# Optimization experiments

Measured on AMD Instinct MI355X. Metric: run time of the kernel, lower is better.

## Reference

```python
import jax, jax.numpy as jnp
import numpy as np
from jax import lax

DEPTH, HEADS, DH, DIM, M, V, NUM_EMB, D_VQ = 6, 8, 64, 512, 256, 523, 512, 64


def _ln(x, g, b):
    mu = jnp.mean(x, -1, keepdims=True)
    var = jnp.var(x, -1, keepdims=True)
    return (x - mu) * lax.rsqrt(var + 1e-5) * g + b


def _softmax_kernel(data, proj, is_query):
    # FAVOR+ positive softmax features (performer-pytorch softmax_kernel)
    dn = data * (data.shape[-1] ** -0.25)
    dd = jnp.einsum('bhld,md->bhlm', dn, proj)
    diag = 0.5 * jnp.sum(dn * dn, axis=-1, keepdims=True)
    mx = jnp.max(dd, axis=-1, keepdims=True) if is_query else jnp.max(dd)
    return jnp.exp(dd - diag - lax.stop_gradient(mx)) * (proj.shape[0] ** -0.5) + 1e-4


def _causal_linear_attn(qp, kp, v):
    # out_t = qp_t . cumsum_t(kp v^T) / (qp_t . cumsum_t(kp))
    kc = jnp.cumsum(kp, axis=2)
    den = jnp.einsum('bhlm,bhlm->bhl', qp, kc)
    kv = jnp.cumsum(jnp.einsum('bhlm,bhld->bhlmd', kp, v), axis=2)
    return jnp.einsum('bhlm,bhlmd->bhld', qp, kv) / den[..., None]


def _vq_encode(_x, conv1_w, conv1_b, conv2_w, conv2_b, codebook):
    dn = ('NCDHW', 'OIDHW', 'NCDHW')
    h = lax.conv_general_dilated(_x, conv1_w, (2, 2, 2), [(1, 1)] * 3, dimension_numbers=dn)
    h = jax.nn.relu(h + conv1_b[None, :, None, None, None])
    h = lax.conv_general_dilated(h, conv2_w, (2, 2, 2), [(1, 1)] * 3, dimension_numbers=dn)
    h = h + conv2_b[None, :, None, None, None]                 # [N, D, 4,4,4]
    z = jnp.transpose(h, (0, 2, 3, 4, 1))                      # [N, 4,4,4, D]
    flat = z.reshape(-1, z.shape[-1])
    d2 = (jnp.sum(flat * flat, 1, keepdims=True)
          - 2.0 * flat @ codebook.T
          + jnp.sum(codebook * codebook, 1)[None, :])
    inds = jnp.argmin(d2, axis=1).astype(jnp.int32)
    return inds.reshape(z.shape[:4])                           # [N, 4,4,4]


def _performer_loss(seq, tok_emb, pos_emb, proj, ln1_g, ln1_b, wq, wk, wv, wo, bo,
                    ln2_g, ln2_b, ff1_w, ff1_b, ff2_w, ff2_b, lnf_g, lnf_b,
                    logits_w, logits_b):
    inp, tgt = seq[:, :-1], seq[:, 1:]
    b, L = inp.shape
    h = tok_emb[inp] + pos_emb[:L][None]
    split = lambda t: jnp.transpose(t.reshape(b, L, HEADS, DH), (0, 2, 1, 3))
    for l in range(DEPTH):
        x1 = _ln(h, ln1_g[l], ln1_b[l])
        q, k, v = split(x1 @ wq[l]), split(x1 @ wk[l]), split(x1 @ wv[l])
        qp = _softmax_kernel(q, proj[l], True)
        kp = _softmax_kernel(k, proj[l], False)
        o = _causal_linear_attn(qp, kp, v)
        o = jnp.transpose(o, (0, 2, 1, 3)).reshape(b, L, DIM)
        h = h + o @ wo[l] + bo[l]
        x2 = _ln(h, ln2_g[l], ln2_b[l])
        h = h + jax.nn.gelu(x2 @ ff1_w[l] + ff1_b[l]) @ ff2_w[l] + ff2_b[l]
    h = _ln(h, lnf_g, lnf_b)
    logits = h @ logits_w + logits_b
    lp = jax.nn.log_softmax(logits, axis=-1)
    nll = -jnp.take_along_axis(lp, tgt[..., None], axis=-1)[..., 0]
    return jnp.mean(nll)


def setup_inputs() -> dict:
    key = jax.random.key(0)
    ks = jax.random.split(key, 24)
    n = lambda k, sh, s=0.02: (jax.random.normal(k, sh) * s).astype(jnp.float32)
    bs = 16
    return {
        'x': jax.random.normal(ks[0], (bs, 1, 16, 16, 16), jnp.float32),
        'xn': jax.random.normal(ks[1], (bs, 1, 1, 16, 16, 16), jnp.float32),
        'i': jax.random.randint(ks[2], (bs, 3), 0, V, jnp.int32),
        # frozen VQ-VAE
        'conv1_w': n(ks[3], (32, 1, 4, 4, 4), 0.1), 'conv1_b': jnp.zeros((32,), jnp.float32),
        'conv2_w': n(ks[4], (D_VQ, 32, 4, 4, 4), 0.05), 'conv2_b': jnp.zeros((D_VQ,), jnp.float32),
        'codebook': jax.random.normal(ks[5], (NUM_EMB, D_VQ), jnp.float32),
        # FAVOR+ random-feature projections (non-trainable buffer)
        'proj': jax.random.normal(ks[6], (DEPTH, M, DH), jnp.float32),
        # performer params
        'tok_emb': n(ks[7], (V, DIM)), 'pos_emb': n(ks[8], (131, DIM)),
        'ln1_g': jnp.ones((DEPTH, DIM), jnp.float32), 'ln1_b': jnp.zeros((DEPTH, DIM), jnp.float32),
        'wq': n(ks[9], (DEPTH, DIM, DIM)), 'wk': n(ks[10], (DEPTH, DIM, DIM)),
        'wv': n(ks[11], (DEPTH, DIM, DIM)), 'wo': n(ks[12], (DEPTH, DIM, DIM)),
        'bo': jnp.zeros((DEPTH, DIM), jnp.float32),
        'ln2_g': jnp.ones((DEPTH, DIM), jnp.float32), 'ln2_b': jnp.zeros((DEPTH, DIM), jnp.float32),
        'ff1_w': n(ks[13], (DEPTH, DIM, 4 * DIM)), 'ff1_b': jnp.zeros((DEPTH, 4 * DIM), jnp.float32),
        'ff2_w': n(ks[14], (DEPTH, 4 * DIM, DIM)), 'ff2_b': jnp.zeros((DEPTH, DIM), jnp.float32),
        'lnf_g': jnp.ones((DIM,), jnp.float32), 'lnf_b': jnp.zeros((DIM,), jnp.float32),
        'logits_w': n(ks[15], (DIM, V)), 'logits_b': jnp.zeros((V,), jnp.float32),
    }


def reference(x, xn, i, conv1_w, conv1_b, conv2_w, conv2_b, codebook, proj,
              tok_emb, pos_emb, ln1_g, ln1_b, wq, wk, wv, wo, bo, ln2_g, ln2_b,
              ff1_w, ff1_b, ff2_w, ff2_b, lnf_g, lnf_b, logits_w, logits_b):
    bs = x.shape[0]
    _xn = xn.reshape((-1,) + xn.shape[2:])            # (b n) c x y z
    _x = jnp.concatenate([x, _xn], axis=0)
    inds = _vq_encode(_x, conv1_w, conv1_b, conv2_w, conv2_b, codebook)
    inds_i = inds[:bs].reshape(bs, -1)                # b (x y z)
    inds_r = inds[bs:].reshape(bs, -1)                # b (n x y z)
    seq = jnp.concatenate([i.astype(jnp.int32), inds_r, inds_i], axis=1)  # [b, 131]
    return _performer_loss(seq, tok_emb, pos_emb, proj, ln1_g, ln1_b, wq, wk, wv, wo,
                           bo, ln2_g, ln2_b, ff1_w, ff1_b, ff2_w, ff2_b,
                           lnf_g, lnf_b, logits_w, logits_b)
```

## Files before the change

kernel.cpp:

```cpp
#include <hip/hip_runtime.h>

#define SEQL 130
#define LSEQ 131
#define DIMM 512
#define NHEADS 8
#define MF 256
#define VSZ 523
#define NROWS (16*SEQL)
#define NBH (16*NHEADS)
#define NBHL (NBH*SEQL)
#define QSEG 1064960

typedef __attribute__((ext_vector_type(8))) short short8;
typedef __attribute__((ext_vector_type(8))) unsigned short us8;
typedef __attribute__((ext_vector_type(4))) unsigned short us4;
typedef __attribute__((ext_vector_type(4))) float f32x4;

__device__ __forceinline__ unsigned short f2bf(float f){
  unsigned int u = __float_as_uint(f);
  u += 0x7fffu + ((u>>16)&1u);
  return (unsigned short)(u>>16);
}
__device__ __forceinline__ float bf2f(unsigned short h){
  return __uint_as_float(((unsigned int)h)<<16);
}
__device__ __forceinline__ float gelu_f(float x){
  float x3 = x*x*x;
  return 0.5f*x*(1.f+tanhf(0.7978845608028654f*(x+0.044715f*x3)));
}
__device__ __forceinline__ unsigned enc_max(float f){
  unsigned u = __float_as_uint(f);
  return (u & 0x80000000u) ? ~u : (u | 0x80000000u);
}
__device__ __forceinline__ float dec_max(unsigned k){
  unsigned u = (k>>31) ? (k & 0x7fffffffu) : ~k;
  return __uint_as_float(u);
}
__device__ __forceinline__ float blk_sum(float v){
  #pragma unroll
  for(int off=32;off;off>>=1) v += __shfl_xor(v,off);
  __shared__ float tmp_s[4];
  int t=threadIdx.x;
  if((t&63)==0) tmp_s[t>>6]=v;
  __syncthreads();
  v = tmp_s[0]+tmp_s[1]+tmp_s[2]+tmp_s[3];
  __syncthreads();
  return v;
}
__device__ __forceinline__ float blk_max(float v){
  #pragma unroll
  for(int off=32;off;off>>=1) v = fmaxf(v,__shfl_xor(v,off));
  __shared__ float tmp_m[4];
  int t=threadIdx.x;
  if((t&63)==0) tmp_m[t>>6]=v;
  __syncthreads();
  v = fmaxf(fmaxf(tmp_m[0],tmp_m[1]),fmaxf(tmp_m[2],tmp_m[3]));
  __syncthreads();
  return v;
}
__device__ __forceinline__ int tok_at(const int* __restrict__ iarr,
    const int* __restrict__ inds, int b, int p){
  if(p<3)  return iarr[b*3+p];
  if(p<67) return inds[(16+b)*64 + (p-3)];
  return inds[b*64 + (p-67)];
}

__global__ __launch_bounds__(256) void conv1_k(const float* __restrict__ x,
    const float* __restrict__ xn, const float* __restrict__ w,
    const float* __restrict__ bias, float* __restrict__ out){
  int idx = blockIdx.x*256 + threadIdx.x;
  if(idx >= 32*32*8*8*8) return;
  int ow = idx & 7, oh = (idx>>3)&7, od = (idx>>6)&7, oc = (idx>>9)&31, n = idx>>14;
  const float* xp = (n<16) ? (x + n*4096) : (xn + (n-16)*4096);
  const float* wp = w + oc*64;
  float acc = bias[oc];
  #pragma unroll
  for(int kd=0;kd<4;kd++){ int id = od*2-1+kd; if((unsigned)id>=16u) continue;
    #pragma unroll
    for(int kh=0;kh<4;kh++){ int ih = oh*2-1+kh; if((unsigned)ih>=16u) continue;
      #pragma unroll
      for(int kw=0;kw<4;kw++){ int iw = ow*2-1+kw; if((unsigned)iw>=16u) continue;
        acc += xp[(id*16+ih)*16+iw]*wp[(kd*4+kh)*4+kw];
      }}}
  out[idx] = fmaxf(acc,0.f);
}

__global__ __launch_bounds__(512) void conv2_k(const float* __restrict__ c1,
    const float* __restrict__ w, const float* __restrict__ bias,
    float* __restrict__ out){
  __shared__ float in_s[32][4][120];
  int od = blockIdx.x, n = blockIdx.y, ocg = blockIdx.z;
  int t = threadIdx.x;
  float4* zf = (float4*)&in_s[0][0][0];
  #pragma unroll
  for(int j=0;j<8;j++){
    int idx = t + 512*j;
    if(idx < 3840) zf[idx] = make_float4(0.f,0.f,0.f,0.f);
  }
  __syncthreads();
  #pragma unroll
  for(int j=0;j<2;j++){
    int ridx = t + 512*j;
    int ic = ridx>>5, rem = ridx&31;
    int kd = rem>>3, ih = rem&7;
    int id = od*2 - 1 + kd;
    if((unsigned)id < 8u){
      const float* src = c1 + (size_t)(n*32+ic)*512 + id*64 + ih*8;
      float4 a = *(const float4*)src;
      float4 b = *(const float4*)(src+4);
      float* dst = &in_s[ic][kd][(ih+1)*12 + 1];
      dst[0]=a.x; dst[1]=a.y; dst[2]=a.z; dst[3]=a.w;
      dst[4]=b.x; dst[5]=b.y; dst[6]=b.z; dst[7]=b.w;
    }
  }
  __syncthreads();
  int oc = ocg*32 + (t>>4);
  int oh = (t>>2)&3, ow = t&3;
  float acc = bias[oc];
  for(int ic=0; ic<32; ic++){
    #pragma unroll
    for(int kd=0;kd<4;kd++){
      #pragma unroll
      for(int kh=0;kh<4;kh++){
        f32x4 wv = *(const f32x4*)(w + ((size_t)(oc*32+ic)*64 + (kd*4+kh)*4));
        const float* base = &in_s[ic][kd][(oh*2+kh)*12 + ow*2];
        acc += wv[0]*base[0] + wv[1]*base[1] + wv[2]*base[2] + wv[3]*base[3];
      }
    }
  }
  out[(size_t)(n*64+oc)*64 + od*16 + oh*4 + ow] = acc;
}

__global__ __launch_bounds__(256) void vq_k(const float* __restrict__ c2,
    const float* __restrict__ cb, int* __restrict__ inds){
  int nf = blockIdx.x;
  int nb = nf>>6, sp = nf&63;
  __shared__ float z[64];
  int t = threadIdx.x;
  if(t<64) z[t] = c2[(nb*64+t)*64 + sp];
  __syncthreads();
  float best = 3.0e38f; int bi = 0;
  for(int j=t; j<512; j+=256){
    const float* cr = cb + j*64;
    float dot=0.f, nn=0.f;
    #pragma unroll 8
    for(int d=0;d<64;d++){ float cv=cr[d]; dot += z[d]*cv; nn += cv*cv; }
    float dist = nn - 2.f*dot;
    if(dist < best){ best=dist; bi=j; }
  }
  #pragma unroll
  for(int off=32;off;off>>=1){
    float ob = __shfl_down(best,off); int oi = __shfl_down(bi,off);
    if(ob<best || (ob==best && oi<bi)){ best=ob; bi=oi; }
  }
  __shared__ float rb[4]; __shared__ int ri[4];
  if((t&63)==0){ rb[t>>6]=best; ri[t>>6]=bi; }
  __syncthreads();
  if(t==0){
    for(int wv=1;wv<4;wv++){ if(rb[wv]<best || (rb[wv]==best && ri[wv]<bi)){ best=rb[wv]; bi=ri[wv]; } }
    inds[nf]=bi;
  }
}

__global__ __launch_bounds__(256) void embed_k(const int* __restrict__ iarr,
    const int* __restrict__ inds, const float* __restrict__ tok,
    const float* __restrict__ pos, float* __restrict__ h){
  int idx = blockIdx.x*256 + threadIdx.x;
  int c = idx & 511; int row = idx >> 9;
  int b = row/SEQL, l = row - b*SEQL;
  int tk = tok_at(iarr, inds, b, l);
  h[idx] = tok[tk*DIMM + c] + pos[l*DIMM + c];
}

__global__ __launch_bounds__(256) void ln_k(const float* __restrict__ in,
    const float* __restrict__ g, const float* __restrict__ bb,
    unsigned short* __restrict__ out){
  int row = blockIdx.x; int t = threadIdx.x;
  const float* xr = in + (size_t)row*DIMM;
  float x0 = xr[t], x1 = xr[t+256];
  float s = x0+x1, ss = x0*x0 + x1*x1;
  #pragma unroll
  for(int off=32;off;off>>=1){ s += __shfl_xor(s,off); ss += __shfl_xor(ss,off); }
  __shared__ float bs[4], bss[4];
  if((t&63)==0){ bs[t>>6]=s; bss[t>>6]=ss; }
  __syncthreads();
  s = bs[0]+bs[1]+bs[2]+bs[3]; ss = bss[0]+bss[1]+bss[2]+bss[3];
  float mu = s*(1.f/512.f);
  float var = ss*(1.f/512.f) - mu*mu;
  float inv = rsqrtf(var + 1e-5f);
  out[(size_t)row*DIMM+t]     = f2bf((x0-mu)*inv*g[t]     + bb[t]);
  out[(size_t)row*DIMM+t+256] = f2bf((x1-mu)*inv*g[t+256] + bb[t+256]);
}

__global__ __launch_bounds__(256) void wprep_k(const float* __restrict__ wq_l,
    const float* __restrict__ wk_l, const float* __restrict__ wv_l,
    const float* __restrict__ wo_l, const float* __restrict__ ff1_l,
    const float* __restrict__ ff2_l,
    unsigned short* __restrict__ wqkvt, unsigned short* __restrict__ wot,
    unsigned short* __restrict__ ff1t, unsigned short* __restrict__ ff2t,
    unsigned int* __restrict__ gmaxbits){
  int bid = blockIdx.x;
  int t = threadIdx.x;
  if(bid==0 && t==0) gmaxbits[0] = 0u;
  const float* src; unsigned short* dst;
  int n0, k0, srcN, dstK;
  if(bid < 768){
    int nt = bid % 48, kt = bid / 48;
    n0 = nt*32; k0 = kt*32;
    int seg = n0 >> 9;
    src = (seg==0 ? wq_l : seg==1 ? wk_l : wv_l);
    dst = wqkvt; srcN = 512; dstK = 512;
  } else if(bid < 1024){
    int b2 = bid-768; int nt = b2 % 16, kt = b2 / 16;
    n0 = nt*32; k0 = kt*32; src = wo_l; dst = wot; srcN = 512; dstK = 512;
  } else if(bid < 2048){
    int b2 = bid-1024; int nt = b2 % 64, kt = b2 / 64;
    n0 = nt*32; k0 = kt*32; src = ff1_l; dst = ff1t; srcN = 2048; dstK = 512;
  } else {
    int b2 = bid-2048; int nt = b2 % 16, kt = b2 / 16;
    n0 = nt*32; k0 = kt*32; src = ff2_l; dst = ff2t; srcN = 512; dstK = 2048;
  }
  int srcCol0 = (bid < 768) ? (n0 & 0x1ff) : n0;
  __shared__ float tile[32][33];
  int c = t&31, r = t>>5;
  #pragma unroll
  for(int j=0;j<4;j++)
    tile[r+8*j][c] = src[(size_t)(k0+r+8*j)*srcN + srcCol0 + c];
  __syncthreads();
  #pragma unroll
  for(int j=0;j<4;j++){
    int n = n0 + r + 8*j;
    dst[(size_t)n*dstK + k0 + c] = f2bf(tile[c][r+8*j]);
  }
}

__global__ __launch_bounds__(256) void wconv_k(const float* __restrict__ W,
    unsigned short* __restrict__ dst, int K, int N){
  __shared__ float tile[32][33];
  int k0 = blockIdx.y*32, n0 = blockIdx.x*32;
  int t = threadIdx.x; int c = t&31, r = t>>5;
  #pragma unroll
  for(int j=0;j<4;j++){
    int n = n0+c;
    tile[r+8*j][c] = (n<N) ? W[(size_t)(k0+r+8*j)*N + n] : 0.f;
  }
  __syncthreads();
  #pragma unroll
  for(int j=0;j<4;j++){
    int n = n0 + r + 8*j;
    if(n<N) dst[(size_t)n*K + k0 + c] = f2bf(tile[c][r+8*j]);
  }
}

__global__ __launch_bounds__(256) void projcv_k(const float* __restrict__ proj,
    unsigned short* __restrict__ pb){
  int i = blockIdx.x*256 + threadIdx.x;
  if(i < 6*MF*64) pb[i] = f2bf(proj[i]);
}

template<int MODE>
__global__ __launch_bounds__(256) void mgemm_k(const unsigned short* __restrict__ A,
    const unsigned short* __restrict__ Bt, const float* __restrict__ bias,
    float* __restrict__ Cf, unsigned short* __restrict__ Cb,
    int M, int N, int K){
  __shared__ unsigned short As[4096];
  __shared__ unsigned short Bs[4096];
  int t = threadIdx.x;
  const int m0 = blockIdx.y*64, n0 = blockIdx.x*64;
  int w = t>>6, l = t&63;
  int wr = w>>1, wc = w&1;
  f32x4 acc[2][2] = {};
  int srow = t>>2, sp = (t&3)*2;
  int arow = m0 + srow, brow = n0 + srow;
  bool aok = arow < M, bok = brow < N;
  const us8* Ap = (const us8*)(A + (size_t)arow*K + sp*8);
  const us8* Bp = (const us8*)(Bt + (size_t)brow*K + sp*8);
  unsigned short* Aw0 = As + srow*64 + (((sp  )^(srow&7))<<3);
  unsigned short* Aw1 = As + srow*64 + (((sp+1)^(srow&7))<<3);
  unsigned short* Bw0 = Bs + srow*64 + (((sp  )^(srow&7))<<3);
  unsigned short* Bw1 = Bs + srow*64 + (((sp+1)^(srow&7))<<3);
  for(int k0=0; k0<K; k0+=64){
    us8 a0={}, a1={}, b0={}, b1={};
    if(aok){ a0 = Ap[0]; a1 = Ap[1]; }
    if(bok){ b0 = Bp[0]; b1 = Bp[1]; }
    Ap += 8; Bp += 8;
    __syncthreads();
    *(us8*)Aw0 = a0; *(us8*)Aw1 = a1;
    *(us8*)Bw0 = b0; *(us8*)Bw1 = b1;
    __syncthreads();
    #pragma unroll
    for(int kk=0;kk<2;kk++){
      short8 af[2], bf[2];
      #pragma unroll
      for(int m=0;m<2;m++){
        int row = wr*32 + m*16 + (l&15);
        int slot = kk*4 + (l>>4);
        af[m] = *(const short8*)(As + row*64 + ((slot^(row&7))<<3));
      }
      #pragma unroll
      for(int n=0;n<2;n++){
        int col = wc*32 + n*16 + (l&15);
        int slot = kk*4 + (l>>4);
        bf[n] = *(const short8*)(Bs + col*64 + ((slot^(col&7))<<3));
      }
      #pragma unroll
      for(int m=0;m<2;m++)
        #pragma unroll
        for(int n=0;n<2;n++)
          acc[m][n] = __builtin_amdgcn_mfma_f32_16x16x32_bf16(af[m], bf[n], acc[m][n], 0, 0, 0);
    }
  }
  #pragma unroll
  for(int m=0;m<2;m++){
    #pragma unroll
    for(int n=0;n<2;n++){
      int col = n0 + wc*32 + n*16 + (l&15);
      #pragma unroll
      for(int i=0;i<4;i++){
        int row = m0 + wr*32 + m*16 + (l>>4)*4 + i;
        if(row < M && col < N){
          float v = acc[m][n][i];
          if(MODE==0){
            if(bias) v += bias[col];
            Cf[(size_t)row*N+col] = v;
          } else if(MODE==1){
            v *= (col < 1024) ? 0.35355339059327378f : 1.0f;
            int seg = col>>9, d0 = col&511;
            int hh = d0>>6, d = d0&63;
            int bb = row/SEQL, ll = row - bb*SEQL;
            Cb[(size_t)seg*QSEG + (((size_t)(bb*NHEADS+hh))*SEQL + ll)*64 + d] = f2bf(v);
          } else if(MODE==3){
            v += bias[col];
            Cf[(size_t)row*N+col] += v;
          } else {
            v += bias[col];
            v = gelu_f(v);
            Cb[(size_t)row*N+col] = f2bf(v);
          }
        }
      }
    }
  }
}

__global__ __launch_bounds__(256) void mgemm32_k(const unsigned short* __restrict__ A,
    const unsigned short* __restrict__ Bt, const float* __restrict__ bias,
    float* __restrict__ Cf, int N, int K){
  __shared__ unsigned short As[2048];
  __shared__ unsigned short Bs[4096];
  int t = threadIdx.x;
  const int m0 = blockIdx.y*32, n0 = blockIdx.x*64;
  int w = t>>6, l = t&63;
  int wm = w&1, wn2 = w>>1;
  f32x4 acc[2] = {};
  int srowA = t>>3, spA = t&7;
  int srowB = t>>2, spB = (t&3)*2;
  const us8* Ap = (const us8*)(A + (size_t)(m0+srowA)*K + spA*8);
  const us8* Bp = (const us8*)(Bt + (size_t)(n0+srowB)*K + spB*8);
  unsigned short* Aw  = As + srowA*64 + ((spA^(srowA&7))<<3);
  unsigned short* Bw0 = Bs + srowB*64 + (((spB  )^(srowB&7))<<3);
  unsigned short* Bw1 = Bs + srowB*64 + (((spB+1)^(srowB&7))<<3);
  for(int k0=0; k0<K; k0+=64){
    us8 a0 = Ap[0];
    us8 b0 = Bp[0], b1 = Bp[1];
    Ap += 8; Bp += 8;
    __syncthreads();
    *(us8*)Aw = a0;
    *(us8*)Bw0 = b0; *(us8*)Bw1 = b1;
    __syncthreads();
    #pragma unroll
    for(int kk=0;kk<2;kk++){
      int arow = wm*16 + (l&15);
      int slot = kk*4 + (l>>4);
      short8 af = *(const short8*)(As + arow*64 + ((slot^(arow&7))<<3));
      #pragma unroll
      for(int n=0;n<2;n++){
        int col = (wn2*2+n)*16 + (l&15);
        short8 bf = *(const short8*)(Bs + col*64 + ((slot^(col&7))<<3));
        acc[n] = __builtin_amdgcn_mfma_f32_16x16x32_bf16(af, bf, acc[n], 0, 0, 0);
      }
    }
  }
  #pragma unroll
  for(int n=0;n<2;n++){
    int col = n0 + (wn2*2+n)*16 + (l&15);
    float bv = bias[col];
    #pragma unroll
    for(int i=0;i<4;i++){
      int row = m0 + wm*16 + (l>>4)*4 + i;
      Cf[(size_t)row*N+col] += acc[n][i] + bv;
    }
  }
}

__global__ __launch_bounds__(256) void featA_k(const unsigned short* __restrict__ qn,
    const unsigned short* __restrict__ kn, const unsigned short* __restrict__ projl,
    unsigned short* __restrict__ qp, unsigned int* __restrict__ gmaxbits){
  int z = blockIdx.y;
  const unsigned short* dn = z ? kn : qn;
  __shared__ float uni[32*264];
  __shared__ unsigned short dns[2048];
  unsigned short* ps = (unsigned short*)uni;
  int t = threadIdx.x;
  size_t R0 = (size_t)blockIdx.x*32;
  {
    int row = t>>3, sl = t&7;
    us8 u = *(const us8*)(dn + (R0+row)*64 + sl*8);
    *(us8*)(dns + row*64 + ((sl^(row&7))<<3)) = u;
  }
  #pragma unroll
  for(int j=0;j<8;j++){
    int ridx = t + 256*j;
    int row = ridx>>3, sl = ridx&7;
    us8 u = *(const us8*)(projl + row*64 + sl*8);
    *(us8*)(ps + row*64 + ((sl^(row&7))<<3)) = u;
  }
  __syncthreads();
  int w = t>>6, l = t&63;
  int rt = w&1, cb = (w>>1)*8;
  f32x4 acc[8] = {};
  #pragma unroll
  for(int kk=0;kk<2;kk++){
    int ar = rt*16 + (l&15);
    int slot = kk*4 + (l>>4);
    short8 a = *(const short8*)(dns + ar*64 + ((slot^(ar&7))<<3));
    #pragma unroll
    for(int ct=0;ct<8;ct++){
      int br = (cb+ct)*16 + (l&15);
      short8 b = *(const short8*)(ps + br*64 + ((slot^(br&7))<<3));
      acc[ct] = __builtin_amdgcn_mfma_f32_16x16x32_bf16(a, b, acc[ct], 0, 0, 0);
    }
  }
  __syncthreads();
  #pragma unroll
  for(int ct=0;ct<8;ct++){
    int col = (cb+ct)*16 + (l&15);
    #pragma unroll
    for(int i=0;i<4;i++){
      int row = rt*16 + (l>>4)*4 + i;
      uni[row*264 + col] = acc[ct][i];
    }
  }
  __syncthreads();
  int r = t>>3, sub = t&7;
  float* rowp = uni + r*264 + sub*32;
  f32x4 v[8];
  #pragma unroll
  for(int jj=0;jj<8;jj++) v[jj] = *(const f32x4*)(rowp + jj*4);
  float m = -3.0e38f;
  #pragma unroll
  for(int jj=0;jj<8;jj++)
    #pragma unroll
    for(int i=0;i<4;i++) m = fmaxf(m, v[jj][i]);
  m = fmaxf(m, __shfl_xor(m,1));
  m = fmaxf(m, __shfl_xor(m,2));
  m = fmaxf(m, __shfl_xor(m,4));
  if(z==0){
    us8 dvu = *(const us8*)(dns + r*64 + ((sub^(r&7))<<3));
    float s2 = 0.f;
    #pragma unroll
    for(int j=0;j<8;j++){ float xx = bf2f(dvu[j]); s2 += xx*xx; }
    s2 += __shfl_xor(s2,1); s2 += __shfl_xor(s2,2); s2 += __shfl_xor(s2,4);
    float ds = 0.5f*s2;
    unsigned short* op = qp + (R0+r)*256 + sub*32;
    #pragma unroll
    for(int jj=0;jj<8;jj++){
      us4 u4;
      #pragma unroll
      for(int i=0;i<4;i++) u4[i] = f2bf(expf(v[jj][i] - ds - m)*0.0625f + 1e-4f);
      *(us4*)(op + jj*4) = u4;
    }
  } else {
    float bm = m;
    bm = fmaxf(bm, __shfl_xor(bm,8));
    bm = fmaxf(bm, __shfl_xor(bm,16));
    bm = fmaxf(bm, __shfl_xor(bm,32));
    __shared__ float wm[4];
    if(l==0) wm[w] = bm;
    __syncthreads();
    if(t==0){
      float g = fmaxf(fmaxf(wm[0],wm[1]),fmaxf(wm[2],wm[3]));
      atomicMax(gmaxbits, enc_max(g));
    }
  }
}

__global__ __launch_bounds__(256) void featB_k(const unsigned short* __restrict__ kn,
    const unsigned short* __restrict__ projl, const unsigned int* __restrict__ gmaxbits,
    unsigned short* __restrict__ kp){
  __shared__ float uni[32*264];
  __shared__ unsigned short dns[2048];
  unsigned short* ps = (unsigned short*)uni;
  int t = threadIdx.x;
  size_t R0 = (size_t)blockIdx.x*32;
  {
    int row = t>>3, sl = t&7;
    us8 u = *(const us8*)(kn + (R0+row)*64 + sl*8);
    *(us8*)(dns + row*64 + ((sl^(row&7))<<3)) = u;
  }
  #pragma unroll
  for(int j=0;j<8;j++){
    int ridx = t + 256*j;
    int row = ridx>>3, sl = ridx&7;
    us8 u = *(const us8*)(projl + row*64 + sl*8);
    *(us8*)(ps + row*64 + ((sl^(row&7))<<3)) = u;
  }
  __syncthreads();
  int w = t>>6, l = t&63;
  int rt = w&1, cb = (w>>1)*8;
  f32x4 acc[8] = {};
  #pragma unroll
  for(int kk=0;kk<2;kk++){
    int ar = rt*16 + (l&15);
    int slot = kk*4 + (l>>4);
    short8 a = *(const short8*)(dns + ar*64 + ((slot^(ar&7))<<3));
    #pragma unroll
    for(int ct=0;ct<8;ct++){
      int br = (cb+ct)*16 + (l&15);
      short8 b = *(const short8*)(ps + br*64 + ((slot^(br&7))<<3));
      acc[ct] = __builtin_amdgcn_mfma_f32_16x16x32_bf16(a, b, acc[ct], 0, 0, 0);
    }
  }
  __syncthreads();
  #pragma unroll
  for(int ct=0;ct<8;ct++){
    int col = (cb+ct)*16 + (l&15);
    #pragma unroll
    for(int i=0;i<4;i++){
      int row = rt*16 + (l>>4)*4 + i;
      uni[row*264 + col] = acc[ct][i];
    }
  }
  __syncthreads();
  float g = dec_max(gmaxbits[0]);
  int r = t>>3, sub = t&7;
  us8 dvu = *(const us8*)(dns + r*64 + ((sub^(r&7))<<3));
  float s2 = 0.f;
  #pragma unroll
  for(int j=0;j<8;j++){ float xx = bf2f(dvu[j]); s2 += xx*xx; }
  s2 += __shfl_xor(s2,1); s2 += __shfl_xor(s2,2); s2 += __shfl_xor(s2,4);
  float ds = 0.5f*s2;
  float* rowp = uni + r*264 + sub*32;
  unsigned short* op = kp + (R0+r)*256 + sub*32;
  #pragma unroll
  for(int jj=0;jj<8;jj++){
    f32x4 v = *(const f32x4*)(rowp + jj*4);
    us4 u4;
    #pragma unroll
    for(int i=0;i<4;i++) u4[i] = f2bf(expf(v[i] - ds - g)*0.0625f + 1e-4f);
    *(us4*)(op + jj*4) = u4;
  }
}

__global__ __launch_bounds__(256) void attn_k(const unsigned short* __restrict__ qp,
    const unsigned short* __restrict__ kp, const unsigned short* __restrict__ vn,
    unsigned short* __restrict__ ob){
  int qt = blockIdx.x, bh = blockIdx.y;
  int b = bh>>3, hh = bh&7;
  __shared__ unsigned short qs[32*256];
  __shared__ unsigned short ks[32*256];
  __shared__ float vs[32][68];
  __shared__ float Ss[32][33];
  __shared__ float dens[2][32];
  int t = threadIdx.x;
  int w = t>>6, l = t&63;
  int qh = w>>1, kh = w&1;
  {
    int rr = t>>3, s0 = (t&7)*4;
    int gr = qt*32 + rr;
    const us8* src = (const us8*)(qp + ((size_t)bh*SEQL + (gr<SEQL?gr:0))*256 + s0*8);
    #pragma unroll
    for(int j=0;j<4;j++){
      us8 u = {};
      if(gr<SEQL) u = src[j];
      *(us8*)(qs + rr*256 + (((s0+j)^(rr&7))<<3)) = u;
    }
  }
  if(t<64) dens[t>>5][t&31] = 0.f;
  float o[8] = {0.f,0.f,0.f,0.f,0.f,0.f,0.f,0.f};
  int orow = t>>3, od = (t&7)*8;
  for(int kt=0; kt<=qt; kt++){
    __syncthreads();
    {
      int rr = t>>3, s0 = (t&7)*4;
      int gk = kt*32 + rr;
      const us8* src = (const us8*)(kp + ((size_t)bh*SEQL + (gk<SEQL?gk:0))*256 + s0*8);
      #pragma unroll
      for(int j=0;j<4;j++){
        us8 u = {};
        if(gk<SEQL) u = src[j];
        *(us8*)(ks + rr*256 + (((s0+j)^(rr&7))<<3)) = u;
      }
      const us8* vsrc = (const us8*)(vn + ((size_t)bh*SEQL + (gk<SEQL?gk:0))*64 + od);
      us8 uv = {};
      if(gk<SEQL) uv = vsrc[0];
      #pragma unroll
      for(int i=0;i<8;i++) vs[rr][od+i] = bf2f(uv[i]);
    }
    __syncthreads();
    f32x4 sacc = {};
    #pragma unroll
    for(int kk=0;kk<8;kk++){
      int ar = qh*16 + (l&15); int slot = kk*4 + (l>>4);
      short8 a = *(const short8*)(qs + ar*256 + ((slot^(ar&7))<<3));
      int br = kh*16 + (l&15);
      short8 bb2 = *(const short8*)(ks + br*256 + ((slot^(br&7))<<3));
      sacc = __builtin_amdgcn_mfma_f32_16x16x32_bf16(a, bb2, sacc, 0, 0, 0);
    }
    int scol = kh*16 + (l&15);
    int gcol = kt*32 + scol;
    float dp[4];
    #pragma unroll
    for(int i=0;i<4;i++){
      int sr = qh*16 + (l>>4)*4 + i;
      int grw = qt*32 + sr;
      float v2 = sacc[i];
      if(gcol > grw) v2 = 0.f;
      Ss[sr][scol] = v2;
      dp[i] = v2;
    }
    #pragma unroll
    for(int off=1;off<16;off<<=1)
      #pragma unroll
      for(int i=0;i<4;i++) dp[i] += __shfl_xor(dp[i], off);
    if((l&15)==0){
      #pragma unroll
      for(int i=0;i<4;i++) dens[kh][qh*16 + (l>>4)*4 + i] += dp[i];
    }
    __syncthreads();
    #pragma unroll
    for(int k2=0;k2<32;k2++){
      float s = Ss[orow][k2];
      #pragma unroll
      for(int j=0;j<8;j++) o[j] += s*vs[k2][od+j];
    }
  }
  __syncthreads();
  int gr = qt*32 + orow;
  if(gr < SEQL){
    float inv = 1.f/(dens[0][orow] + dens[1][orow]);
    us8 u;
    #pragma unroll
    for(int j=0;j<8;j++) u[j] = f2bf(o[j]*inv);
    *(us8*)(ob + ((size_t)(b*SEQL+gr))*DIMM + hh*64 + od) = u;
  }
}

__global__ __launch_bounds__(256) void loss_k(const float* __restrict__ logits,
    const int* __restrict__ iarr, const int* __restrict__ inds,
    float* __restrict__ rnll){
  int row = blockIdx.x; int t = threadIdx.x;
  const float* lr = logits + (size_t)row*VSZ;
  float m = -3.0e38f;
  for(int j=t;j<VSZ;j+=256) m = fmaxf(m, lr[j]);
  m = blk_max(m);
  float s = 0.f;
  for(int j=t;j<VSZ;j+=256) s += expf(lr[j]-m);
  s = blk_sum(s);
  if(t==0){
    int b = row/SEQL, l = row - b*SEQL;
    int tgt = tok_at(iarr, inds, b, l+1);
    rnll[row] = (m + logf(s)) - lr[tgt];
  }
}

__global__ __launch_bounds__(256) void fin_k(const float* __restrict__ rnll,
    float* __restrict__ out){
  int t = threadIdx.x;
  float s = 0.f;
  for(int i=t;i<NROWS;i+=256) s += rnll[i];
  s = blk_sum(s);
  if(t==0) out[0] = s/(float)NROWS;
}

extern "C" void kernel_launch(void* const* d_in, const int* in_sizes, int n_in,
                              void* d_out, int out_size, void* d_ws, size_t ws_size,
                              hipStream_t stream){
  (void)in_sizes; (void)n_in; (void)out_size; (void)ws_size;
  const float* x        = (const float*)d_in[0];
  const float* xn       = (const float*)d_in[1];
  const int*   iarr     = (const int*)  d_in[2];
  const float* conv1_w  = (const float*)d_in[3];
  const float* conv1_b  = (const float*)d_in[4];
  const float* conv2_w  = (const float*)d_in[5];
  const float* conv2_b  = (const float*)d_in[6];
  const float* codebook = (const float*)d_in[7];
  const float* proj     = (const float*)d_in[8];
  const float* tok_emb  = (const float*)d_in[9];
  const float* pos_emb  = (const float*)d_in[10];
  const float* ln1_g    = (const float*)d_in[11];
  const float* ln1_b    = (const float*)d_in[12];
  const float* wq       = (const float*)d_in[13];
  const float* wk       = (const float*)d_in[14];
  const float* wv       = (const float*)d_in[15];
  const float* wo       = (const float*)d_in[16];
  const float* bo       = (const float*)d_in[17];
  const float* ln2_g    = (const float*)d_in[18];
  const float* ln2_b    = (const float*)d_in[19];
  const float* ff1_w    = (const float*)d_in[20];
  const float* ff1_b    = (const float*)d_in[21];
  const float* ff2_w    = (const float*)d_in[22];
  const float* ff2_b    = (const float*)d_in[23];
  const float* lnf_g    = (const float*)d_in[24];
  const float* lnf_b    = (const float*)d_in[25];
  const float* logits_w = (const float*)d_in[26];
  const float* logits_b = (const float*)d_in[27];

  float* wsf = (float*)d_ws;
  size_t off = 0;
  unsigned short* qp_bf = (unsigned short*)(wsf + off); off += 2129920;
  unsigned short* kp_bf = (unsigned short*)(wsf + off); off += 2129920;
  float* h = wsf + off; off += 1064960;
  unsigned short* x1b = (unsigned short*)(wsf + off); off += 532480;
  unsigned short* qkvb = (unsigned short*)(wsf + off); off += 1597440;
  unsigned short* ob  = (unsigned short*)(wsf + off); off += 532480;
  unsigned short* projb = (unsigned short*)(wsf + off); off += 49152;
  unsigned short* wqkvt = (unsigned short*)(wsf + off); off += 393216;
  unsigned short* wot   = (unsigned short*)(wsf + off); off += 131072;
  unsigned short* ff1t  = (unsigned short*)(wsf + off); off += 524288;
  unsigned short* ff2t  = (unsigned short*)(wsf + off); off += 524288;
  unsigned short* logt  = (unsigned short*)(wsf + off); off += 133888;
  unsigned short* ffmid = (unsigned short*)(wsf + off); off += 2129920;
  float* logits = wsf + off; off += 1087840;
  int* inds = (int*)(wsf + off); off += 2048;
  unsigned int* gmaxbits = (unsigned int*)(wsf + off); off += 64;
  float* rnll = wsf + off; off += 2112;

  float* c1 = (float*)ffmid;
  float* c2 = ((float*)ffmid) + 524288;

  unsigned short* qnb = qkvb;
  unsigned short* knb = qkvb + QSEG;
  unsigned short* vnb = qkvb + 2*QSEG;

  conv1_k<<<2048,256,0,stream>>>(x, xn, conv1_w, conv1_b, c1);
  conv2_k<<<dim3(4,32,2),512,0,stream>>>(c1, conv2_w, conv2_b, c2);
  vq_k<<<2048,256,0,stream>>>(c2, codebook, inds);
  embed_k<<<(NROWS*DIMM)/256,256,0,stream>>>(iarr, inds, tok_emb, pos_emb, h);
  projcv_k<<<384,256,0,stream>>>(proj, projb);
  wconv_k<<<dim3(17,16),256,0,stream>>>(logits_w, logt, 512, 523);

  for(int l=0;l<6;l++){
    wprep_k<<<3072,256,0,stream>>>(wq + (size_t)l*262144, wk + (size_t)l*262144,
        wv + (size_t)l*262144, wo + (size_t)l*262144,
        ff1_w + (size_t)l*1048576, ff2_w + (size_t)l*1048576,
        wqkvt, wot, ff1t, ff2t, gmaxbits);
    ln_k<<<NROWS,256,0,stream>>>(h, ln1_g+l*DIMM, ln1_b+l*DIMM, x1b);
    mgemm_k<1><<<dim3(24,33),256,0,stream>>>(x1b, wqkvt, nullptr, nullptr, qkvb, NROWS, 1536, DIMM);
    featA_k<<<dim3(520,2),256,0,stream>>>(qnb, knb, projb + l*16384, qp_bf, gmaxbits);
    featB_k<<<520,256,0,stream>>>(knb, projb + l*16384, gmaxbits, kp_bf);
    attn_k<<<dim3(5,NBH),256,0,stream>>>(qp_bf, kp_bf, vnb, ob);
    mgemm32_k<<<dim3(8,65),256,0,stream>>>(ob, wot, bo+l*DIMM, h, DIMM, DIMM);
    ln_k<<<NROWS,256,0,stream>>>(h, ln2_g+l*DIMM, ln2_b+l*DIMM, x1b);
    mgemm_k<4><<<dim3(32,33),256,0,stream>>>(x1b, ff1t, ff1_b+l*2048, nullptr, ffmid, NROWS, 2048, DIMM);
    mgemm32_k<<<dim3(8,65),256,0,stream>>>(ffmid, ff2t, ff2_b+l*DIMM, h, DIMM, 2048);
  }

  ln_k<<<NROWS,256,0,stream>>>(h, lnf_g, lnf_b, x1b);
  mgemm_k<0><<<dim3(9,33),256,0,stream>>>(x1b, logt, logits_b, logits, nullptr, NROWS, VSZ, DIMM);
  loss_k<<<NROWS,256,0,stream>>>(logits, iarr, inds, rnll);
  fin_k<<<1,256,0,stream>>>(rnll, (float*)d_out);
}
```

Before: 796.0 us.

## Replace direct conv2 with im2col plus bf16 MFMA GEMM

The scalar direct conv2 kernel is replaced by three steps: an im2col kernel that writes bf16 patches, a bf16 conversion of the conv2 weights, and the existing MFMA GEMM, now templated to store rather than accumulate. The output lands in a spatial-major layout, so the VQ kernel reads contiguous vectors. The proj conversion moves to a shared 8-wide vectorized convert kernel. This adds extra launches and an im2col buffer, and rounding conv2 inputs to bf16 could change argmin choices in the VQ step.

New measurement: 787.7 us. Within noise of the previous version (-1.0%).

```diff
diff --git a/kernel.cpp b/kernel.cpp
--- a/kernel.cpp
+++ b/kernel.cpp
@@ -85,66 +85,54 @@
   out[idx] = fmaxf(acc,0.f);
 }
 
-__global__ __launch_bounds__(512) void conv2_k(const float* __restrict__ c1,
-    const float* __restrict__ w, const float* __restrict__ bias,
-    float* __restrict__ out){
-  __shared__ float in_s[32][4][120];
-  int od = blockIdx.x, n = blockIdx.y, ocg = blockIdx.z;
-  int t = threadIdx.x;
-  float4* zf = (float4*)&in_s[0][0][0];
-  #pragma unroll
-  for(int j=0;j<8;j++){
-    int idx = t + 512*j;
-    if(idx < 3840) zf[idx] = make_float4(0.f,0.f,0.f,0.f);
-  }
-  __syncthreads();
-  #pragma unroll
-  for(int j=0;j<2;j++){
-    int ridx = t + 512*j;
-    int ic = ridx>>5, rem = ridx&31;
-    int kd = rem>>3, ih = rem&7;
-    int id = od*2 - 1 + kd;
-    if((unsigned)id < 8u){
-      const float* src = c1 + (size_t)(n*32+ic)*512 + id*64 + ih*8;
-      float4 a = *(const float4*)src;
-      float4 b = *(const float4*)(src+4);
-      float* dst = &in_s[ic][kd][(ih+1)*12 + 1];
-      dst[0]=a.x; dst[1]=a.y; dst[2]=a.z; dst[3]=a.w;
-      dst[4]=b.x; dst[5]=b.y; dst[6]=b.z; dst[7]=b.w;
-    }
-  }
-  __syncthreads();
-  int oc = ocg*32 + (t>>4);
-  int oh = (t>>2)&3, ow = t&3;
-  float acc = bias[oc];
-  for(int ic=0; ic<32; ic++){
-    #pragma unroll
-    for(int kd=0;kd<4;kd++){
-      #pragma unroll
-      for(int kh=0;kh<4;kh++){
-        f32x4 wv = *(const f32x4*)(w + ((size_t)(oc*32+ic)*64 + (kd*4+kh)*4));
-        const float* base = &in_s[ic][kd][(oh*2+kh)*12 + ow*2];
-        acc += wv[0]*base[0] + wv[1]*base[1] + wv[2]*base[2] + wv[3]*base[3];
-      }
-    }
-  }
-  out[(size_t)(n*64+oc)*64 + od*16 + oh*4 + ow] = acc;
-}
-
-__global__ __launch_bounds__(256) void vq_k(const float* __restrict__ c2,
+__global__ __launch_bounds__(256) void cvt8_k(const float* __restrict__ src,
+    unsigned short* __restrict__ dst, int n8){
+  int i = blockIdx.x*256 + threadIdx.x;
+  if(i >= n8) return;
+  const float* s = src + (size_t)i*8;
+  us8 u;
+  #pragma unroll
+  for(int j=0;j<8;j++) u[j] = f2bf(s[j]);
+  *(us8*)(dst + (size_t)i*8) = u;
+}
+
+__global__ __launch_bounds__(256) void im2col_k(const float* __restrict__ c1,
+    unsigned short* __restrict__ icol){
+  int tid = blockIdx.x*256 + threadIdx.x;
+  size_t e0 = (size_t)tid*8;
+  int r = (int)(e0 >> 11);
+  int k0 = (int)(e0 & 2047);
+  int n = r>>6, od = (r>>4)&3, oh = (r>>2)&3, ow = r&3;
+  int ic = k0>>6, kd = (k0>>4)&3, kh0 = (k0>>2)&3;
+  int id = od*2 - 1 + kd;
+  us8 u = {};
+  if((unsigned)id < 8u){
+    const float* base = c1 + (size_t)(n*32+ic)*512 + id*64;
+    #pragma unroll
+    for(int j=0;j<8;j++){
+      int kh = kh0 + (j>>2), kw = j&3;
+      int ih = oh*2 - 1 + kh, iw = ow*2 - 1 + kw;
+      float v = 0.f;
+      if((unsigned)ih < 8u && (unsigned)iw < 8u) v = base[ih*8 + iw];
+      u[j] = f2bf(v);
+    }
+  }
+  *(us8*)(icol + e0) = u;
+}
+
+__global__ __launch_bounds__(256) void vq_k(const float* __restrict__ z,
     const float* __restrict__ cb, int* __restrict__ inds){
   int nf = blockIdx.x;
-  int nb = nf>>6, sp = nf&63;
-  __shared__ float z[64];
+  __shared__ float zs[64];
   int t = threadIdx.x;
-  if(t<64) z[t] = c2[(nb*64+t)*64 + sp];
+  if(t<64) zs[t] = z[(size_t)nf*64 + t];
   __syncthreads();
   float best = 3.0e38f; int bi = 0;
   for(int j=t; j<512; j+=256){
     const float* cr = cb + j*64;
     float dot=0.f, nn=0.f;
     #pragma unroll 8
-    for(int d=0;d<64;d++){ float cv=cr[d]; dot += z[d]*cv; nn += cv*cv; }
+    for(int d=0;d<64;d++){ float cv=cr[d]; dot += zs[d]*cv; nn += cv*cv; }
     float dist = nn - 2.f*dot;
     if(dist < best){ best=dist; bi=j; }
   }
@@ -250,12 +238,6 @@
     int n = n0 + r + 8*j;
     if(n<N) dst[(size_t)n*K + k0 + c] = f2bf(tile[c][r+8*j]);
   }
-}
-
-__global__ __launch_bounds__(256) void projcv_k(const float* __restrict__ proj,
-    unsigned short* __restrict__ pb){
-  int i = blockIdx.x*256 + threadIdx.x;
-  if(i < 6*MF*64) pb[i] = f2bf(proj[i]);
 }
 
 template<int MODE>
@@ -343,6 +325,7 @@
   }
 }
 
+template<int ACC>
 __global__ __launch_bounds__(256) void mgemm32_k(const unsigned short* __restrict__ A,
     const unsigned short* __restrict__ Bt, const float* __restrict__ bias,
     float* __restrict__ Cf, int N, int K){
@@ -388,7 +371,8 @@
     #pragma unroll
     for(int i=0;i<4;i++){
       int row = m0 + wm*16 + (l>>4)*4 + i;
-      Cf[(size_t)row*N+col] += acc[n][i] + bv;
+      if(ACC) Cf[(size_t)row*N+col] += acc[n][i] + bv;
+      else    Cf[(size_t)row*N+col]  = acc[n][i] + bv;
     }
   }
 }
@@ -726,18 +710,22 @@
   unsigned int* gmaxbits = (unsigned int*)(wsf + off); off += 64;
   float* rnll = wsf + off; off += 2112;
 
-  float* c1 = (float*)ffmid;
-  float* c2 = ((float*)ffmid) + 524288;
+  float* c1 = logits;
+  unsigned short* icol = ffmid;
+  float* zbuf = (float*)qp_bf;
+  unsigned short* cw2b = (unsigned short*)kp_bf;
 
   unsigned short* qnb = qkvb;
   unsigned short* knb = qkvb + QSEG;
   unsigned short* vnb = qkvb + 2*QSEG;
 
   conv1_k<<<2048,256,0,stream>>>(x, xn, conv1_w, conv1_b, c1);
-  conv2_k<<<dim3(4,32,2),512,0,stream>>>(c1, conv2_w, conv2_b, c2);
-  vq_k<<<2048,256,0,stream>>>(c2, codebook, inds);
+  cvt8_k<<<64,256,0,stream>>>(conv2_w, cw2b, 16384);
+  im2col_k<<<2048,256,0,stream>>>(c1, icol);
+  mgemm32_k<0><<<dim3(1,64),256,0,stream>>>(icol, cw2b, conv2_b, zbuf, 64, 2048);
+  vq_k<<<2048,256,0,stream>>>(zbuf, codebook, inds);
   embed_k<<<(NROWS*DIMM)/256,256,0,stream>>>(iarr, inds, tok_emb, pos_emb, h);
-  projcv_k<<<384,256,0,stream>>>(proj, projb);
+  cvt8_k<<<48,256,0,stream>>>(proj, projb, 12288);
   wconv_k<<<dim3(17,16),256,0,stream>>>(logits_w, logt, 512, 523);
 
   for(int l=0;l<6;l++){
@@ -750,10 +738,10 @@
     featA_k<<<dim3(520,2),256,0,stream>>>(qnb, knb, projb + l*16384, qp_bf, gmaxbits);
     featB_k<<<520,256,0,stream>>>(knb, projb + l*16384, gmaxbits, kp_bf);
     attn_k<<<dim3(5,NBH),256,0,stream>>>(qp_bf, kp_bf, vnb, ob);
-    mgemm32_k<<<dim3(8,65),256,0,stream>>>(ob, wot, bo+l*DIMM, h, DIMM, DIMM);
+    mgemm32_k<1><<<dim3(8,65),256,0,stream>>>(ob, wot, bo+l*DIMM, h, DIMM, DIMM);
     ln_k<<<NROWS,256,0,stream>>>(h, ln2_g+l*DIMM, ln2_b+l*DIMM, x1b);
     mgemm_k<4><<<dim3(32,33),256,0,stream>>>(x1b, ff1t, ff1_b+l*2048, nullptr, ffmid, NROWS, 2048, DIMM);
-    mgemm32_k<<<dim3(8,65),256,0,stream>>>(ffmid, ff2t, ff2_b+l*DIMM, h, DIMM, 2048);
+    mgemm32_k<1><<<dim3(8,65),256,0,stream>>>(ffmid, ff2t, ff2_b+l*DIMM, h, DIMM, 2048);
   }
 
   ln_k<<<NROWS,256,0,stream>>>(h, lnf_g, lnf_b, x1b);
```
